# Kernel optimization log

Measured on AMD Instinct MI355X. Metric: run time of the kernel, lower is better.

Reference implementation:

```python
import jax, jax.numpy as jnp
import numpy as np

def setup_inputs() -> dict:
    key = jax.random.key(0)
    k1, k2, k3 = jax.random.split(key, 3)
    shape = (2, 2048, 8, 64)  # [n, l, h, d]
    return {
        "q": jax.random.normal(k1, shape, dtype=jnp.float32),
        "k": jax.random.normal(k2, shape, dtype=jnp.float32),
        "v": jax.random.normal(k3, shape, dtype=jnp.float32),
    }

def reference(q, k, v):
    # QK^T: [n, l, s, h]
    qk = jnp.einsum('nlhd,nshd->nlsh', q, k)
    softmax_temp = 1.0 / (q.shape[3] ** 0.5)
    attn = jax.nn.softmax(softmax_temp * qk, axis=2)
    # weighted values: [n, l, h, d]
    return jnp.einsum('nlsh,nshd->nlhd', attn, v)
```

## Files before the change

### kernel.cpp

```cpp
#include <hip/hip_runtime.h>
#include <hip/hip_bf16.h>
#include <math.h>

typedef float floatx4 __attribute__((ext_vector_type(4)));
typedef __bf16 bf16x8 __attribute__((ext_vector_type(8)));

#define SEQ 2048
#define NH 8
#define DH 64
#define NB 2
#define HEADS 16
#define HSTRIDE (SEQ * DH)
#define TILE_E (64 * 64)

__device__ __forceinline__ unsigned short f2bf(float x) {
  union { __bf16 b; unsigned short u; } c; c.b = (__bf16)x; return c.u;
}
__device__ __forceinline__ unsigned int pk2bf(float a, float b) {
  union { __hip_bfloat162 h2; unsigned int u; } c;
  c.h2 = __float22bfloat162_rn(make_float2(a, b));
  return c.u;
}

__global__ __launch_bounds__(256)
void pack_kv(const float* __restrict__ k, const float* __restrict__ v,
             unsigned short* __restrict__ kb, unsigned short* __restrict__ vb) {
  __shared__ unsigned short Ts[64][68];
  const int tid  = threadIdx.x;
  const int bx   = blockIdx.x;
  const int kt   = bx & 31;
  const int head = bx >> 5;
  const int n = head >> 3, h = head & 7;

  #pragma unroll
  for (int j2 = 0; j2 < 2; ++j2) {
    int c = j2 * 256 + tid;
    int t2f = c >> 6, lane = c & 63;
    int l16 = lane & 15, quad = lane >> 4;
    int t = t2f >> 1, f = t2f & 1;
    int s = kt * 64 + t * 16 + l16;
    const float* src = k + ((size_t)(n * SEQ + s) * NH + h) * DH + f * 32 + quad * 8;
    float4 a = *(const float4*)src;
    float4 b = *(const float4*)(src + 4);
    ushort4 lo, hi;
    lo.x = f2bf(a.x); lo.y = f2bf(a.y); lo.z = f2bf(a.z); lo.w = f2bf(a.w);
    hi.x = f2bf(b.x); hi.y = f2bf(b.y); hi.z = f2bf(b.z); hi.w = f2bf(b.w);
    unsigned short* dst = kb + (size_t)head * HSTRIDE + kt * TILE_E + c * 8;
    *(ushort4*)dst = lo;
    *(ushort4*)(dst + 4) = hi;
  }

  #pragma unroll
  for (int i = 0; i < 4; ++i) {
    int id = i * 256 + tid;
    int s  = id >> 4;
    int c4 = (id & 15) * 4;
    size_t g = ((size_t)((n * SEQ + kt * 64 + s) * NH + h)) * DH + c4;
    float4 x = *(const float4*)(v + g);
    ushort4 y;
    y.x = f2bf(x.x); y.y = f2bf(x.y); y.z = f2bf(x.z); y.w = f2bf(x.w);
    *(ushort4*)&Ts[s][c4] = y;
  }
  __syncthreads();
  #pragma unroll
  for (int j2 = 0; j2 < 2; ++j2) {
    int c = j2 * 256 + tid;
    int h4t = c >> 6, lane = c & 63;
    int l16 = lane & 15, quad = lane >> 4;
    int half = h4t >> 2, t = h4t & 3;
    int d = t * 16 + l16;
    int s0 = half * 32 + quad * 8;
    ushort4 lo, hi;
    lo.x = Ts[s0 + 0][d]; lo.y = Ts[s0 + 1][d]; lo.z = Ts[s0 + 2][d]; lo.w = Ts[s0 + 3][d];
    hi.x = Ts[s0 + 4][d]; hi.y = Ts[s0 + 5][d]; hi.z = Ts[s0 + 6][d]; hi.w = Ts[s0 + 7][d];
    unsigned short* dst = vb + (size_t)head * HSTRIDE + kt * TILE_E + c * 8;
    *(ushort4*)dst = lo;
    *(ushort4*)(dst + 4) = hi;
  }
}

#define SMEM_BYTES 36864

__global__ __launch_bounds__(512)
void attn(const float* __restrict__ q, const unsigned short* __restrict__ kb,
          const unsigned short* __restrict__ vt, float* __restrict__ out) {
  __shared__ __align__(16) char smem[SMEM_BYTES];
  unsigned short* Pw = (unsigned short*)smem;
  float* oM = (float*)smem;
  float* lM = (float*)(smem + 8 * 16 * 68 * 4);

  const int tid  = threadIdx.x;
  const int wave = tid >> 6;
  const int lane = tid & 63;
  const int quad = lane >> 4;
  const int l16  = lane & 15;

  const int bx   = blockIdx.x;
  const int head = bx & 15;
  const int qg   = bx >> 4;
  const int n = head >> 3, h = head & 7;

  const unsigned short* kf = kb + (size_t)head * HSTRIDE;
  const unsigned short* vf = vt + (size_t)head * HSTRIDE;

  bf16x8 aq[4][2];
  #pragma unroll
  for (int msub = 0; msub < 4; ++msub)
    #pragma unroll
    for (int f = 0; f < 2; ++f) {
      const float* src = q + ((size_t)((n * SEQ + qg * 64 + msub * 16 + l16) * NH + h)) * DH
                         + f * 32 + quad * 8;
      float4 x0 = *(const float4*)src;
      float4 x1 = *(const float4*)(src + 4);
      union { unsigned int u32[4]; bf16x8 v8; } u;
      u.u32[0] = pk2bf(x0.x, x0.y); u.u32[1] = pk2bf(x0.z, x0.w);
      u.u32[2] = pk2bf(x1.x, x1.y); u.u32[3] = pk2bf(x1.z, x1.w);
      aq[msub][f] = u.v8;
    }

  floatx4 o[4][4];
  float lsum[4];
  #pragma unroll
  for (int msub = 0; msub < 4; ++msub) {
    #pragma unroll
    for (int t = 0; t < 4; ++t) o[msub][t] = floatx4{0.f, 0.f, 0.f, 0.f};
    lsum[msub] = 0.f;
  }

  const float S = 0.125f * 1.4426950408889634f;
  const float C = 12.0f;

  for (int it = 0; it < 4; ++it) {
    const unsigned short* kbase = kf + (it * 8 + wave) * TILE_E;
    const unsigned short* vbase = vf + (it * 8 + wave) * TILE_E;

    bf16x8 bk[4][2];
    #pragma unroll
    for (int t = 0; t < 4; ++t)
      #pragma unroll
      for (int f = 0; f < 2; ++f)
        bk[t][f] = *(const bf16x8*)(kbase + ((t * 2 + f) * 64 + lane) * 8);
    bf16x8 bv[2][4];
    #pragma unroll
    for (int half = 0; half < 2; ++half)
      #pragma unroll
      for (int t = 0; t < 4; ++t)
        bv[half][t] = *(const bf16x8*)(vbase + ((half * 4 + t) * 64 + lane) * 8);

    floatx4 acc2[2][4];
    #pragma unroll
    for (int t = 0; t < 4; ++t) {
      acc2[0][t] = floatx4{0.f, 0.f, 0.f, 0.f};
      acc2[0][t] = __builtin_amdgcn_mfma_f32_16x16x32_bf16(bk[t][0], aq[0][0], acc2[0][t], 0, 0, 0);
      acc2[0][t] = __builtin_amdgcn_mfma_f32_16x16x32_bf16(bk[t][1], aq[0][1], acc2[0][t], 0, 0, 0);
    }

    #pragma unroll
    for (int m = 0; m < 4; ++m) {
      const int cb = m & 1;
      unsigned short* pb = Pw + (wave * 2 + cb) * 16 * 72;

      #pragma unroll
      for (int t = 0; t < 4; ++t) {
        float p0 = __builtin_amdgcn_exp2f(acc2[cb][t][0] * S - C);
        float p1 = __builtin_amdgcn_exp2f(acc2[cb][t][1] * S - C);
        float p2 = __builtin_amdgcn_exp2f(acc2[cb][t][2] * S - C);
        float p3 = __builtin_amdgcn_exp2f(acc2[cb][t][3] * S - C);
        lsum[m] += (p0 + p1) + (p2 + p3);
        uint2 pk; pk.x = pk2bf(p0, p1); pk.y = pk2bf(p2, p3);
        *(uint2*)(pb + l16 * 72 + t * 16 + quad * 4) = pk;
      }

      if (m < 3) {
        #pragma unroll
        for (int t = 0; t < 4; ++t) {
          acc2[cb ^ 1][t] = floatx4{0.f, 0.f, 0.f, 0.f};
          acc2[cb ^ 1][t] = __builtin_amdgcn_mfma_f32_16x16x32_bf16(bk[t][0], aq[m + 1][0], acc2[cb ^ 1][t], 0, 0, 0);
          acc2[cb ^ 1][t] = __builtin_amdgcn_mfma_f32_16x16x32_bf16(bk[t][1], aq[m + 1][1], acc2[cb ^ 1][t], 0, 0, 0);
        }
      }

      #pragma unroll
      for (int half = 0; half < 2; ++half) {
        bf16x8 a = *(const bf16x8*)(pb + l16 * 72 + half * 32 + quad * 8);
        #pragma unroll
        for (int t = 0; t < 4; ++t)
          o[m][t] = __builtin_amdgcn_mfma_f32_16x16x32_bf16(a, bv[half][t], o[m][t], 0, 0, 0);
      }
    }
  }

  #pragma unroll
  for (int msub = 0; msub < 4; ++msub) {
    float s = lsum[msub];
    s += __shfl_xor(s, 16, 64);
    s += __shfl_xor(s, 32, 64);
    lsum[msub] = s;
  }

  const int mrow = tid >> 5;
  const int mcol = (tid & 31) * 2;
  #pragma unroll
  for (int p = 0; p < 4; ++p) {
    __syncthreads();
    #pragma unroll
    for (int t = 0; t < 4; ++t)
      #pragma unroll
      for (int r = 0; r < 4; ++r)
        oM[(wave * 16 + quad * 4 + r) * 68 + t * 16 + l16] = o[p][t][r];
    if (quad == 0) lM[wave * 16 + l16] = lsum[p];
    __syncthreads();
    float v0 = 0.f, v1 = 0.f, l = 0.f;
    #pragma unroll
    for (int w = 0; w < 8; ++w) {
      float2 t2 = *(const float2*)&oM[(w * 16 + mrow) * 68 + mcol];
      v0 += t2.x; v1 += t2.y;
      l += lM[w * 16 + mrow];
    }
    float inv = 1.f / l;
    const int grow = qg * 64 + p * 16 + mrow;
    float2 st; st.x = v0 * inv; st.y = v1 * inv;
    *(float2*)(out + ((size_t)((n * SEQ + grow) * NH + h)) * DH + mcol) = st;
  }
}

extern "C" void kernel_launch(void* const* d_in, const int* in_sizes, int n_in,
                              void* d_out, int out_size, void* d_ws, size_t ws_size,
                              hipStream_t stream) {
  const float* q = (const float*)d_in[0];
  const float* k = (const float*)d_in[1];
  const float* v = (const float*)d_in[2];
  float* out = (float*)d_out;
  (void)in_sizes; (void)n_in; (void)out_size; (void)ws_size;

  unsigned short* kb = (unsigned short*)d_ws;
  unsigned short* vb = kb + (size_t)HEADS * HSTRIDE;

  pack_kv<<<HEADS * (SEQ / 64), 256, 0, stream>>>(k, v, kb, vb);
  attn<<<HEADS * (SEQ / 64), 512, 0, stream>>>(q, kb, vb, out);
}
```

Measured before the change: 104.3 us.

## Switch attention to 32x32x16 MFMA with register-resident P via lane shuffles

Replaces the 16x16x32 bf16 MFMA tiling with 32x32x16 MFMA tiles for both QK^T and PV, and repacks K and V in the pack kernel to match the new operand layout. The softmax probabilities now stay in registers and are rearranged into the A-operand layout with cross-half-wave shuffles, so the LDS round trip for P goes away. This is meant to cut LDS traffic and raise MFMA efficiency, at the cost of larger accumulator register footprints and changes to the epilogue reduction mapping.

```diff
diff --git a/kernel.cpp b/kernel.cpp
--- a/kernel.cpp
+++ b/kernel.cpp
@@ -2,7 +2,7 @@
 #include <hip/hip_bf16.h>
 #include <math.h>
 
-typedef float floatx4 __attribute__((ext_vector_type(4)));
+typedef float floatx16 __attribute__((ext_vector_type(16)));
 typedef __bf16 bf16x8 __attribute__((ext_vector_type(8)));
 
 #define SEQ 2048
@@ -35,11 +35,11 @@
   #pragma unroll
   for (int j2 = 0; j2 < 2; ++j2) {
     int c = j2 * 256 + tid;
-    int t2f = c >> 6, lane = c & 63;
-    int l16 = lane & 15, quad = lane >> 4;
-    int t = t2f >> 1, f = t2f & 1;
-    int s = kt * 64 + t * 16 + l16;
-    const float* src = k + ((size_t)(n * SEQ + s) * NH + h) * DH + f * 32 + quad * 8;
+    int lane = c & 63;
+    int kk = (c >> 6) & 3, ks2 = c >> 8;
+    int row = kt * 64 + ks2 * 32 + (lane & 31);
+    int d0  = kk * 16 + (lane >> 5) * 8;
+    const float* src = k + ((size_t)(n * SEQ + row) * NH + h) * DH + d0;
     float4 a = *(const float4*)src;
     float4 b = *(const float4*)(src + 4);
     ushort4 lo, hi;
@@ -65,11 +65,10 @@
   #pragma unroll
   for (int j2 = 0; j2 < 2; ++j2) {
     int c = j2 * 256 + tid;
-    int h4t = c >> 6, lane = c & 63;
-    int l16 = lane & 15, quad = lane >> 4;
-    int half = h4t >> 2, t = h4t & 3;
-    int d = t * 16 + l16;
-    int s0 = half * 32 + quad * 8;
+    int lane = c & 63;
+    int dsub = (c >> 6) & 1, ss = c >> 7;
+    int s0 = ss * 16 + (lane >> 5) * 8;
+    int d  = dsub * 32 + (lane & 31);
     ushort4 lo, hi;
     lo.x = Ts[s0 + 0][d]; lo.y = Ts[s0 + 1][d]; lo.z = Ts[s0 + 2][d]; lo.w = Ts[s0 + 3][d];
     hi.x = Ts[s0 + 4][d]; hi.y = Ts[s0 + 5][d]; hi.z = Ts[s0 + 6][d]; hi.w = Ts[s0 + 7][d];
@@ -79,21 +78,29 @@
   }
 }
 
-#define SMEM_BYTES 36864
+__device__ __forceinline__ void halfswap(unsigned a, unsigned b, bool lo,
+                                         unsigned& outA, unsigned& outB) {
+  unsigned m = lo ? b : a;
+  unsigned sx = (unsigned)__shfl_xor((int)m, 32, 64);
+  outA = lo ? a : sx;
+  outB = lo ? sx : b;
+}
+
+#define SMEM_BYTES 35328
 
 __global__ __launch_bounds__(512)
 void attn(const float* __restrict__ q, const unsigned short* __restrict__ kb,
           const unsigned short* __restrict__ vt, float* __restrict__ out) {
   __shared__ __align__(16) char smem[SMEM_BYTES];
-  unsigned short* Pw = (unsigned short*)smem;
   float* oM = (float*)smem;
   float* lM = (float*)(smem + 8 * 16 * 68 * 4);
 
   const int tid  = threadIdx.x;
   const int wave = tid >> 6;
   const int lane = tid & 63;
-  const int quad = lane >> 4;
-  const int l16  = lane & 15;
+  const int l32  = lane & 31;
+  const int hl   = lane >> 5;
+  const bool lo  = (hl == 0);
 
   const int bx   = blockIdx.x;
   const int head = bx & 15;
@@ -103,112 +110,106 @@
   const unsigned short* kf = kb + (size_t)head * HSTRIDE;
   const unsigned short* vf = vt + (size_t)head * HSTRIDE;
 
-  bf16x8 aq[4][2];
-  #pragma unroll
-  for (int msub = 0; msub < 4; ++msub)
-    #pragma unroll
-    for (int f = 0; f < 2; ++f) {
-      const float* src = q + ((size_t)((n * SEQ + qg * 64 + msub * 16 + l16) * NH + h)) * DH
-                         + f * 32 + quad * 8;
+  bf16x8 qB[2][4];
+  #pragma unroll
+  for (int qs = 0; qs < 2; ++qs)
+    #pragma unroll
+    for (int kk = 0; kk < 4; ++kk) {
+      const int row = qg * 64 + qs * 32 + l32;
+      const float* src = q + ((size_t)((n * SEQ + row) * NH + h)) * DH + kk * 16 + hl * 8;
       float4 x0 = *(const float4*)src;
       float4 x1 = *(const float4*)(src + 4);
       union { unsigned int u32[4]; bf16x8 v8; } u;
       u.u32[0] = pk2bf(x0.x, x0.y); u.u32[1] = pk2bf(x0.z, x0.w);
       u.u32[2] = pk2bf(x1.x, x1.y); u.u32[3] = pk2bf(x1.z, x1.w);
-      aq[msub][f] = u.v8;
-    }
-
-  floatx4 o[4][4];
-  float lsum[4];
-  #pragma unroll
-  for (int msub = 0; msub < 4; ++msub) {
-    #pragma unroll
-    for (int t = 0; t < 4; ++t) o[msub][t] = floatx4{0.f, 0.f, 0.f, 0.f};
-    lsum[msub] = 0.f;
+      qB[qs][kk] = u.v8;
+    }
+
+  floatx16 o[2][2];
+  float lsum[2];
+  #pragma unroll
+  for (int qs = 0; qs < 2; ++qs) {
+    lsum[qs] = 0.f;
+    #pragma unroll
+    for (int d = 0; d < 2; ++d)
+      #pragma unroll
+      for (int i = 0; i < 16; ++i) o[qs][d][i] = 0.f;
   }
 
   const float S = 0.125f * 1.4426950408889634f;
   const float C = 12.0f;
 
   for (int it = 0; it < 4; ++it) {
-    const unsigned short* kbase = kf + (it * 8 + wave) * TILE_E;
-    const unsigned short* vbase = vf + (it * 8 + wave) * TILE_E;
-
-    bf16x8 bk[4][2];
-    #pragma unroll
-    for (int t = 0; t < 4; ++t)
-      #pragma unroll
-      for (int f = 0; f < 2; ++f)
-        bk[t][f] = *(const bf16x8*)(kbase + ((t * 2 + f) * 64 + lane) * 8);
-    bf16x8 bv[2][4];
-    #pragma unroll
-    for (int half = 0; half < 2; ++half)
-      #pragma unroll
-      for (int t = 0; t < 4; ++t)
-        bv[half][t] = *(const bf16x8*)(vbase + ((half * 4 + t) * 64 + lane) * 8);
-
-    floatx4 acc2[2][4];
-    #pragma unroll
-    for (int t = 0; t < 4; ++t) {
-      acc2[0][t] = floatx4{0.f, 0.f, 0.f, 0.f};
-      acc2[0][t] = __builtin_amdgcn_mfma_f32_16x16x32_bf16(bk[t][0], aq[0][0], acc2[0][t], 0, 0, 0);
-      acc2[0][t] = __builtin_amdgcn_mfma_f32_16x16x32_bf16(bk[t][1], aq[0][1], acc2[0][t], 0, 0, 0);
-    }
-
-    #pragma unroll
-    for (int m = 0; m < 4; ++m) {
-      const int cb = m & 1;
-      unsigned short* pb = Pw + (wave * 2 + cb) * 16 * 72;
-
-      #pragma unroll
-      for (int t = 0; t < 4; ++t) {
-        float p0 = __builtin_amdgcn_exp2f(acc2[cb][t][0] * S - C);
-        float p1 = __builtin_amdgcn_exp2f(acc2[cb][t][1] * S - C);
-        float p2 = __builtin_amdgcn_exp2f(acc2[cb][t][2] * S - C);
-        float p3 = __builtin_amdgcn_exp2f(acc2[cb][t][3] * S - C);
-        lsum[m] += (p0 + p1) + (p2 + p3);
-        uint2 pk; pk.x = pk2bf(p0, p1); pk.y = pk2bf(p2, p3);
-        *(uint2*)(pb + l16 * 72 + t * 16 + quad * 4) = pk;
+    const int kt = it * 8 + wave;
+    const unsigned short* kt_base = kf + kt * TILE_E;
+    const unsigned short* vt_base = vf + kt * TILE_E;
+
+    #pragma unroll
+    for (int ks2 = 0; ks2 < 2; ++ks2) {
+      bf16x8 kA[4];
+      #pragma unroll
+      for (int kk = 0; kk < 4; ++kk)
+        kA[kk] = *(const bf16x8*)(kt_base + ((ks2 * 4 + kk) * 64 + lane) * 8);
+      bf16x8 vB[2][2];
+      #pragma unroll
+      for (int ssl = 0; ssl < 2; ++ssl)
+        #pragma unroll
+        for (int dsub = 0; dsub < 2; ++dsub)
+          vB[ssl][dsub] = *(const bf16x8*)(vt_base + (((ks2 * 2 + ssl) * 2 + dsub) * 64 + lane) * 8);
+
+      #pragma unroll
+      for (int qs = 0; qs < 2; ++qs) {
+        floatx16 acc;
+        #pragma unroll
+        for (int i = 0; i < 16; ++i) acc[i] = 0.f;
+        #pragma unroll
+        for (int kk = 0; kk < 4; ++kk)
+          acc = __builtin_amdgcn_mfma_f32_32x32x16_bf16(kA[kk], qB[qs][kk], acc, 0, 0, 0);
+
+        unsigned pk[8];
+        #pragma unroll
+        for (int g2 = 0; g2 < 4; ++g2) {
+          float p0 = __builtin_amdgcn_exp2f(acc[4 * g2 + 0] * S - C);
+          float p1 = __builtin_amdgcn_exp2f(acc[4 * g2 + 1] * S - C);
+          float p2 = __builtin_amdgcn_exp2f(acc[4 * g2 + 2] * S - C);
+          float p3 = __builtin_amdgcn_exp2f(acc[4 * g2 + 3] * S - C);
+          lsum[qs] += (p0 + p1) + (p2 + p3);
+          pk[g2 * 2]     = pk2bf(p0, p1);
+          pk[g2 * 2 + 1] = pk2bf(p2, p3);
+        }
+
+        union { unsigned u32[4]; bf16x8 v8; } A1, A2;
+        halfswap(pk[0], pk[2], lo, A1.u32[0], A1.u32[2]);
+        halfswap(pk[1], pk[3], lo, A1.u32[1], A1.u32[3]);
+        halfswap(pk[4], pk[6], lo, A2.u32[0], A2.u32[2]);
+        halfswap(pk[5], pk[7], lo, A2.u32[1], A2.u32[3]);
+
+        o[qs][0] = __builtin_amdgcn_mfma_f32_32x32x16_bf16(A1.v8, vB[0][0], o[qs][0], 0, 0, 0);
+        o[qs][1] = __builtin_amdgcn_mfma_f32_32x32x16_bf16(A1.v8, vB[0][1], o[qs][1], 0, 0, 0);
+        o[qs][0] = __builtin_amdgcn_mfma_f32_32x32x16_bf16(A2.v8, vB[1][0], o[qs][0], 0, 0, 0);
+        o[qs][1] = __builtin_amdgcn_mfma_f32_32x32x16_bf16(A2.v8, vB[1][1], o[qs][1], 0, 0, 0);
       }
-
-      if (m < 3) {
-        #pragma unroll
-        for (int t = 0; t < 4; ++t) {
-          acc2[cb ^ 1][t] = floatx4{0.f, 0.f, 0.f, 0.f};
-          acc2[cb ^ 1][t] = __builtin_amdgcn_mfma_f32_16x16x32_bf16(bk[t][0], aq[m + 1][0], acc2[cb ^ 1][t], 0, 0, 0);
-          acc2[cb ^ 1][t] = __builtin_amdgcn_mfma_f32_16x16x32_bf16(bk[t][1], aq[m + 1][1], acc2[cb ^ 1][t], 0, 0, 0);
-        }
-      }
-
-      #pragma unroll
-      for (int half = 0; half < 2; ++half) {
-        bf16x8 a = *(const bf16x8*)(pb + l16 * 72 + half * 32 + quad * 8);
-        #pragma unroll
-        for (int t = 0; t < 4; ++t)
-          o[m][t] = __builtin_amdgcn_mfma_f32_16x16x32_bf16(a, bv[half][t], o[m][t], 0, 0, 0);
-      }
-    }
-  }
-
-  #pragma unroll
-  for (int msub = 0; msub < 4; ++msub) {
-    float s = lsum[msub];
-    s += __shfl_xor(s, 16, 64);
-    s += __shfl_xor(s, 32, 64);
-    lsum[msub] = s;
-  }
+    }
+  }
+
+  #pragma unroll
+  for (int qs = 0; qs < 2; ++qs)
+    lsum[qs] += __shfl_xor(lsum[qs], 32, 64);
 
   const int mrow = tid >> 5;
   const int mcol = (tid & 31) * 2;
   #pragma unroll
   for (int p = 0; p < 4; ++p) {
+    const int qsub = p >> 1, rh = p & 1;
     __syncthreads();
     #pragma unroll
-    for (int t = 0; t < 4; ++t)
-      #pragma unroll
-      for (int r = 0; r < 4; ++r)
-        oM[(wave * 16 + quad * 4 + r) * 68 + t * 16 + l16] = o[p][t][r];
-    if (quad == 0) lM[wave * 16 + l16] = lsum[p];
+    for (int r8 = 0; r8 < 8; ++r8) {
+      const int r   = rh * 8 + r8;
+      const int rip = (r8 & 3) + 4 * hl + 8 * (r8 >> 2);
+      oM[(wave * 16 + rip) * 68 + l32]      = o[qsub][0][r];
+      oM[(wave * 16 + rip) * 68 + 32 + l32] = o[qsub][1][r];
+    }
+    if (lane < 32 && ((lane >> 4) & 1) == rh) lM[wave * 16 + (lane & 15)] = lsum[qsub];
     __syncthreads();
     float v0 = 0.f, v1 = 0.f, l = 0.f;
     #pragma unroll
```

Measured after the change: 107.1 us. +2.7%, slower.
